# Kernel optimization log

Hardware: AMD Instinct MI355X
Metric: run time of the kernel (lower is better)

The kernel has to match this reference:

```python
import jax, jax.numpy as jnp
import numpy as np

EPS = 1e-5
NUM_HEADS = 16
HEAD_DIM = 128


def setup_inputs() -> dict:
    key = jax.random.key(0)
    ks = jax.random.split(key, 9)
    B, S, D = 2, 2048, 2048
    Hd2 = HEAD_DIM // 2
    # rotary angles: proper cos/sin of random phases (unit-modulus freqs_cis)
    theta = jax.random.uniform(ks[1], (B, S, Hd2), jnp.float32, 0.0, 2 * np.pi)
    return {
        "hidden_states": jax.random.normal(ks[0], (B, S, D), jnp.float32),
        "freqs_cos": jnp.cos(theta),
        "freqs_sin": jnp.sin(theta),
        "Wq": jax.random.normal(ks[2], (D, D), jnp.float32) * (D ** -0.5),
        "Wk": jax.random.normal(ks[3], (D, D), jnp.float32) * (D ** -0.5),
        "Wv": jax.random.normal(ks[4], (D, D), jnp.float32) * (D ** -0.5),
        "Wo": jax.random.normal(ks[5], (D, D), jnp.float32) * (D ** -0.5),
        "gq": jnp.ones((HEAD_DIM,), jnp.float32),
        "gk": jnp.ones((HEAD_DIM,), jnp.float32),
    }


def _rmsnorm(x, g):
    # normalize over last (head) dim, eps=1e-5, learned scale
    var = jnp.mean(jnp.square(x), axis=-1, keepdims=True)
    return x * jax.lax.rsqrt(var + EPS) * g


def _rope(x, cos, sin):
    # x: [B,S,H,hd]; treat last dim as hd/2 complex pairs; cos/sin: [B,S,hd/2]
    B, S, H, hd = x.shape
    xp = x.reshape(B, S, H, hd // 2, 2)
    xr, xi = xp[..., 0], xp[..., 1]
    c = cos[:, :, None, :]
    s = sin[:, :, None, :]
    out_r = xr * c - xi * s
    out_i = xr * s + xi * c
    return jnp.stack([out_r, out_i], axis=-1).reshape(B, S, H, hd)


def reference(hidden_states, freqs_cos, freqs_sin, Wq, Wk, Wv, Wo, gq, gk):
    B, S, D = hidden_states.shape
    H, hd = NUM_HEADS, HEAD_DIM
    q = (hidden_states @ Wq).reshape(B, S, H, hd)
    k = (hidden_states @ Wk).reshape(B, S, H, hd)
    v = (hidden_states @ Wv).reshape(B, S, H, hd)
    q = _rmsnorm(q, gq)
    k = _rmsnorm(k, gk)
    q = _rope(q, freqs_cos, freqs_sin)
    k = _rope(k, freqs_cos, freqs_sin)
    scale = 1.0 / np.sqrt(hd)
    scores = jnp.einsum("bqhd,bkhd->bhqk", q, k) * scale
    attn = jax.nn.softmax(scores, axis=-1)
    out = jnp.einsum("bhqk,bkhd->bqhd", attn, v)  # [B,S,H,hd]
    out = out.reshape(B, S, H * hd)
    return out @ Wo
```

## Files before the change

### kernel.cpp

```cpp
#include <hip/hip_runtime.h>
#include <hip/hip_bf16.h>

typedef __attribute__((ext_vector_type(8))) short bf16x8;
typedef __attribute__((ext_vector_type(4))) short bf16x4;
typedef __attribute__((ext_vector_type(4))) float f32x4;
typedef __attribute__((ext_vector_type(16))) float f32x16;
typedef __attribute__((ext_vector_type(4))) int   i32x4;
typedef __attribute__((ext_vector_type(2))) unsigned u32x2;
typedef __attribute__((ext_vector_type(4))) unsigned u32x4;

#define D_MODEL 2048
#define NTOK    4096
#define NH      16
#define HD      128
#define SEQ     2048
#define NQKV    6144

__device__ __forceinline__ short f2bf(float f) {
  unsigned u = __builtin_bit_cast(unsigned, f);
  unsigned r = u + 0x7FFFu + ((u >> 16) & 1u);
  return (short)(r >> 16);
}
__device__ __forceinline__ float bf2f(short s) {
  return __builtin_bit_cast(float, ((unsigned)(unsigned short)s) << 16);
}

__device__ __forceinline__ float exp2fast(float x) {
#if __has_builtin(__builtin_amdgcn_exp2f)
  return __builtin_amdgcn_exp2f(x);
#else
  return exp2f(x);
#endif
}

__device__ __forceinline__ unsigned cvt_pk_bf16(float a, float b) {
  unsigned r;
  asm("v_cvt_pk_bf16_f32 %0, %1, %2" : "=v"(r) : "v"(a), "v"(b));
  return r;
}

__device__ __forceinline__ void permswap(unsigned& x, unsigned& y) {
#if __has_builtin(__builtin_amdgcn_permlane32_swap)
  u32x2 r = __builtin_amdgcn_permlane32_swap(x, y, false, false);
  x = r[0]; y = r[1];
#else
  asm volatile("v_permlane32_swap_b32 %0, %1" : "+v"(x), "+v"(y));
#endif
}

__device__ __forceinline__ f32x16 mfma32(bf16x8 a, bf16x8 b, f32x16 c) {
  return __builtin_amdgcn_mfma_f32_32x32x16_bf16(a, b, c, 0, 0, 0);
}

__device__ __forceinline__ void gload_lds16(const void* g, void* l) {
  typedef __attribute__((address_space(1))) const unsigned gu32;
  typedef __attribute__((address_space(3))) unsigned lu32;
  __builtin_amdgcn_global_load_lds((gu32*)(uintptr_t)g,
                                   (lu32*)(unsigned)(uintptr_t)l, 16, 0, 0);
}

__global__ __launch_bounds__(256) void cast_bf16(const float* __restrict__ in,
                                                 short* __restrict__ out, int n4) {
  int i = blockIdx.x * 256 + threadIdx.x;
  if (i >= n4) return;
  float4 v = ((const float4*)in)[i];
  short4 o;
  o.x = f2bf(v.x); o.y = f2bf(v.y); o.z = f2bf(v.z); o.w = f2bf(v.w);
  ((short4*)out)[i] = o;
}

__global__ __launch_bounds__(256) void wtrans(const float* __restrict__ w0,
                                              const float* __restrict__ w1,
                                              const float* __restrict__ w2,
                                              const float* __restrict__ w3,
                                              short* __restrict__ wt) {
  int z = blockIdx.z;
  const float* W = (z == 0) ? w0 : (z == 1) ? w1 : (z == 2) ? w2 : w3;
  short* O = wt + (size_t)z * D_MODEL * D_MODEL;
  int n0 = blockIdx.x * 64, k0 = blockIdx.y * 64;
  __shared__ short T[64 * 136];
  int tid = threadIdx.x;
#pragma unroll
  for (int it = 0; it < 4; ++it) {
    int f = it * 256 + tid, kk = f >> 4, nc = f & 15;
    float4 v = *(const float4*)&W[(size_t)(k0 + kk) * D_MODEL + n0 + nc * 4];
    short4 o;
    o.x = f2bf(v.x); o.y = f2bf(v.y); o.z = f2bf(v.z); o.w = f2bf(v.w);
    *(short4*)&T[kk * 136 + nc * 4] = o;
  }
  __syncthreads();
#pragma unroll
  for (int it = 0; it < 4; ++it) {
    int u = it * 256 + tid, nn = u >> 4, kc = u & 15;
    short4 o;
    o.x = T[(kc * 4 + 0) * 136 + nn];
    o.y = T[(kc * 4 + 1) * 136 + nn];
    o.z = T[(kc * 4 + 2) * 136 + nn];
    o.w = T[(kc * 4 + 3) * 136 + nn];
    *(short4*)&O[(size_t)(n0 + nn) * D_MODEL + k0 + kc * 4] = o;
  }
}

template <bool OUTBF16>
__global__ __launch_bounds__(512, 4) void gemm8(const short* __restrict__ A,
                                                const short* __restrict__ Bt,
                                                void* __restrict__ Cv, int CS) {
  __shared__ short L[3 * 12288];
  int tid = threadIdx.x, w = tid >> 6, lane = tid & 63, c = lane & 15, g = lane >> 4;

  int gx = gridDim.x, gy = gridDim.y;
  int lin = blockIdx.x + gx * blockIdx.y;
  int idx = lin >> 3, nst = (gx * gy) >> 7;
  int s = (lin & 7) * nst + (idx >> 4);
  int w16 = idx & 15;
  int smR = gy >> 2;
  int mblk = (s % smR) * 4 + (w16 >> 2);
  int nblk = (s / smR) * 4 + (w16 & 3);
  int m0 = mblk * 256, n0 = nblk * 128;
  int wm = w >> 1, wn = w & 1;

  const int NKT = D_MODEL / 32;

  int asrc[2], bsrc;
#pragma unroll
  for (int q = 0; q < 2; ++q) {
    int o = (2 * w + q) * 1024 + lane * 16;
    int os = o ^ (((o >> 7) & 7) << 4);
    asrc[q] = (m0 + (os >> 6)) * D_MODEL + ((os & 63) >> 1);
  }
  {
    int o = w * 1024 + lane * 16;
    int os = o ^ (((o >> 7) & 7) << 4);
    bsrc = (n0 + (os >> 6)) * D_MODEL + ((os & 63) >> 1);
  }

  int aoff[4], boff[4];
#pragma unroll
  for (int mi = 0; mi < 4; ++mi) {
    int r = wm * 64 + mi * 16 + c;
    int o = r * 64 + g * 16;
    aoff[mi] = o ^ (((o >> 7) & 7) << 4);
  }
#pragma unroll
  for (int ni = 0; ni < 4; ++ni) {
    int r = wn * 64 + ni * 16 + c;
    int o = r * 64 + g * 16;
    boff[ni] = 16384 + (o ^ (((o >> 7) & 7) << 4));
  }

  auto STAGE = [&](int jt, int slot) {
    int kk = jt * 32;
    char* base = (char*)L + slot * 24576;
    gload_lds16(A + asrc[0] + kk, base + (2 * w) * 1024);
    gload_lds16(A + asrc[1] + kk, base + (2 * w + 1) * 1024);
    gload_lds16(Bt + bsrc + kk, base + 16384 + w * 1024);
  };

  f32x4 acc[4][4] = {};

  STAGE(0, 0); STAGE(1, 1);
  asm volatile("s_waitcnt vmcnt(3)" ::: "memory");
  __builtin_amdgcn_s_barrier();
  asm volatile("" ::: "memory");

  int rdslot = 0;
  for (int jt = 0; jt < NKT; ++jt) {
    int stslot = rdslot + 2; if (stslot >= 3) stslot -= 3;
    if (jt + 2 < NKT) STAGE(jt + 2, stslot);
    const char* buf = (const char*)L + rdslot * 24576;
    bf16x8 af[4], bfv[4];
#pragma unroll
    for (int mi = 0; mi < 4; ++mi) af[mi] = *(const bf16x8*)(buf + aoff[mi]);
#pragma unroll
    for (int ni = 0; ni < 4; ++ni) bfv[ni] = *(const bf16x8*)(buf + boff[ni]);
    __builtin_amdgcn_s_setprio(1);
#pragma unroll
    for (int mi = 0; mi < 4; ++mi)
#pragma unroll
      for (int ni = 0; ni < 4; ++ni)
        acc[mi][ni] = __builtin_amdgcn_mfma_f32_16x16x32_bf16(af[mi], bfv[ni],
                                                              acc[mi][ni], 0, 0, 0);
    __builtin_amdgcn_s_setprio(0);
    if (jt + 1 < NKT) {
      if (jt + 2 < NKT) { asm volatile("s_waitcnt vmcnt(3)" ::: "memory"); }
      else              { asm volatile("s_waitcnt vmcnt(0)" ::: "memory"); }
      __builtin_amdgcn_s_barrier();
      asm volatile("" ::: "memory");
    }
    rdslot = (rdslot == 2) ? 0 : rdslot + 1;
  }

  int row0 = m0 + wm * 64, col0 = n0 + wn * 64;
  if (OUTBF16) {
    short* Cb = (short*)Cv;
#pragma unroll
    for (int mi = 0; mi < 4; ++mi)
#pragma unroll
      for (int ni = 0; ni < 4; ++ni)
#pragma unroll
        for (int i = 0; i < 4; ++i)
          Cb[(size_t)(row0 + mi * 16 + g * 4 + i) * CS + col0 + ni * 16 + c] =
              f2bf(acc[mi][ni][i]);
  } else {
    float* Cf = (float*)Cv;
#pragma unroll
    for (int mi = 0; mi < 4; ++mi)
#pragma unroll
      for (int ni = 0; ni < 4; ++ni)
#pragma unroll
        for (int i = 0; i < 4; ++i)
          Cf[(size_t)(row0 + mi * 16 + g * 4 + i) * CS + col0 + ni * 16 + c] =
              acc[mi][ni][i];
  }
}

__global__ __launch_bounds__(256) void norm_rope(const short* __restrict__ qkv16,
                                                 const float* __restrict__ cosb,
                                                 const float* __restrict__ sinb,
                                                 const float* __restrict__ gq,
                                                 const float* __restrict__ gk,
                                                 short* __restrict__ qn,
                                                 short* __restrict__ kn) {
  int z = blockIdx.y;
  const float* gg = z ? gk : gq;
  short* O = z ? kn : qn;
  int w = threadIdx.x >> 6, lane = threadIdx.x & 63;
  int p = blockIdx.x * 4 + w;
  int token = p >> 4, h = p & 15;
  int v = *(const int*)&qkv16[(size_t)token * NQKV + z * D_MODEL + h * HD + lane * 2];
  float x0 = bf2f((short)(v & 0xffff));
  float x1 = bf2f((short)((unsigned)v >> 16));
  float ss = x0 * x0 + x1 * x1;
#pragma unroll
  for (int mk = 32; mk; mk >>= 1) ss += __shfl_xor(ss, mk);
  float rs = rsqrtf(ss * (1.f / 128.f) + 1e-5f);
  float qs = z ? 1.0f : 0.12751744f;
  rs *= qs;
  float xr = x0 * rs * gg[lane * 2];
  float xi = x1 * rs * gg[lane * 2 + 1];
  float cc = cosb[(size_t)token * 64 + lane];
  float sn = sinb[(size_t)token * 64 + lane];
  float or_ = xr * cc - xi * sn;
  float oi_ = xr * sn + xi * cc;
  int b = token >> 11, sidx = token & 2047;
  size_t dst = ((size_t)(b * NH + h) * SEQ + sidx) * HD + lane * 2;
  unsigned pk = (unsigned)(unsigned short)f2bf(or_) |
                ((unsigned)(unsigned short)f2bf(oi_) << 16);
  *(unsigned*)&O[dst] = pk;
}

__global__ __launch_bounds__(256) void vtrans(const short* __restrict__ qkv16,
                                              short* __restrict__ vt) {
  int st = blockIdx.x, bh = blockIdx.y;
  int b = bh >> 4, h = bh & 15;
  int t0 = b * SEQ + st * 64;
  __shared__ short Lt[64 * 136];
  int tid = threadIdx.x;
#pragma unroll
  for (int it = 0; it < 4; ++it) {
    int f = it * 256 + tid, tk = f >> 4, ch = f & 15;
    *(i32x4*)&Lt[tk * 136 + ch * 8] =
        *(const i32x4*)&qkv16[(size_t)(t0 + tk) * NQKV + 2 * D_MODEL + h * HD + ch * 8];
  }
  __syncthreads();
#pragma unroll
  for (int it = 0; it < 4; ++it) {
    int u = it * 256 + tid, d = u >> 3, kg = u & 7;
    bf16x8 o;
#pragma unroll
    for (int j = 0; j < 8; ++j) o[j] = Lt[(kg * 8 + j) * 136 + d];
    *(bf16x8*)&vt[(size_t)(bh * HD + d) * SEQ + st * 64 + kg * 8] = o;
  }
}

__global__ __launch_bounds__(512, 2) void flash(const short* __restrict__ qn,
                                                const short* __restrict__ kn,
                                                const short* __restrict__ vt,
                                                short* __restrict__ attn) {
  __shared__ short Ks[2][64 * 128];
  __shared__ short Vs[2][128 * 64];
  int tid = threadIdx.x, w = tid >> 6, lane = tid & 63;
  int q31 = lane & 31, hi = lane >> 5;

  int phys = blockIdx.x;
  int xcd = phys & 7, idx = phys >> 3;
  int bh = xcd * 4 + (idx >> 3);
  int qb = idx & 7;
  int q0 = qb * 256 + w * 32;

  const size_t base = (size_t)bh * SEQ * HD;
  const short* Kg = kn + base;
  const short* Vg = vt + base;

  bf16x8 qf[8];
#pragma unroll
  for (int s = 0; s < 8; ++s)
    qf[s] = *(const bf16x8*)&qn[base + (size_t)(q0 + q31) * HD + s * 16 + hi * 8];

  f32x16 acc[4] = {};
  float m_ = -1e30f, l_ = 0.f;

  int ksrc[2], vsrc[2];
#pragma unroll
  for (int p = 0; p < 2; ++p) {
    int ch = w * 2 + p;
    int o = ch * 1024 + lane * 16;
    int kr = o >> 8, kc = o & 255;
    ksrc[p] = kr * HD + ((kc ^ ((kr & 7) << 4)) >> 1);
    int vr = o >> 7, vc = o & 127;
    vsrc[p] = vr * SEQ + ((vc ^ ((vr & 7) << 4)) >> 1);
  }
  int swz = (q31 & 7) << 4;
  int koff[8], voff[4];
#pragma unroll
  for (int kf = 0; kf < 8; ++kf) koff[kf] = (kf * 32 + hi * 16) ^ swz;
#pragma unroll
  for (int kk = 0; kk < 4; ++kk) voff[kk] = (kk * 32 + hi * 16) ^ swz;
  int krow0 = q31 * 256, krow1 = (32 + q31) * 256;

#pragma unroll
  for (int p = 0; p < 2; ++p) {
    int ch = w * 2 + p;
    gload_lds16(Kg + ksrc[p], (char*)&Ks[0][0] + ch * 1024);
    gload_lds16(Vg + vsrc[p], (char*)&Vs[0][0] + ch * 1024);
  }

  const int NT = SEQ / 64;
  for (int t = 0; t < NT; ++t) {
    int cur = t & 1;
    __syncthreads();
    if (t + 1 < NT) {
      int k0n = (t + 1) * 64;
#pragma unroll
      for (int p = 0; p < 2; ++p) {
        int ch = w * 2 + p;
        gload_lds16(Kg + (size_t)k0n * HD + ksrc[p], (char*)&Ks[cur ^ 1][0] + ch * 1024);
        gload_lds16(Vg + k0n + vsrc[p],              (char*)&Vs[cur ^ 1][0] + ch * 1024);
      }
    }
    const char* Kb = (const char*)&Ks[cur][0];
    const char* Vb = (const char*)&Vs[cur][0];

    f32x16 s0 = {0,0,0,0,0,0,0,0,0,0,0,0,0,0,0,0};
    f32x16 s1 = {0,0,0,0,0,0,0,0,0,0,0,0,0,0,0,0};
    __builtin_amdgcn_s_setprio(1);
#pragma unroll
    for (int kf = 0; kf < 8; ++kf) {
      bf16x8 k0 = *(const bf16x8*)(Kb + krow0 + koff[kf]);
      s0 = mfma32(k0, qf[kf], s0);
      bf16x8 k1 = *(const bf16x8*)(Kb + krow1 + koff[kf]);
      s1 = mfma32(k1, qf[kf], s1);
    }
    __builtin_amdgcn_s_setprio(0);

    float p0 = -1e30f, p1 = -1e30f, p2 = -1e30f, p3 = -1e30f;
#pragma unroll
    for (int i = 0; i < 4; ++i) {
      p0 = fmaxf(p0, fmaxf(s0[i], s0[i + 4]));
      p1 = fmaxf(p1, fmaxf(s0[i + 8], s0[i + 12]));
      p2 = fmaxf(p2, fmaxf(s1[i], s1[i + 4]));
      p3 = fmaxf(p3, fmaxf(s1[i + 8], s1[i + 12]));
    }
    float pmax = fmaxf(fmaxf(p0, p1), fmaxf(p2, p3));
    pmax = fmaxf(pmax, __shfl_xor(pmax, 32));
    if (!__all(pmax <= m_ + 11.5f)) {
      float mn = fmaxf(m_, pmax);
      float al = exp2fast(m_ - mn);
      m_ = mn; l_ *= al;
#pragma unroll
      for (int db = 0; db < 4; ++db)
#pragma unroll
        for (int i = 0; i < 16; ++i) acc[db][i] *= al;
    }
    float r0 = 0.f, r1 = 0.f;
#pragma unroll
    for (int i = 0; i < 16; ++i) {
      float pa = exp2fast(s0[i] - m_); r0 += pa; s0[i] = pa;
      float pb = exp2fast(s1[i] - m_); r1 += pb; s1[i] = pb;
    }
    float r = r0 + r1;
    r += __shfl_xor(r, 32);
    l_ += r;

    __builtin_amdgcn_s_setprio(1);
#pragma unroll
    for (int kt = 0; kt < 2; ++kt) {
      const f32x16& sv = kt ? s1 : s0;
#pragma unroll
      for (int c2 = 0; c2 < 2; ++c2) {
        unsigned x0 = cvt_pk_bf16(sv[c2 * 8 + 0], sv[c2 * 8 + 1]);
        unsigned x1 = cvt_pk_bf16(sv[c2 * 8 + 2], sv[c2 * 8 + 3]);
        unsigned y0 = cvt_pk_bf16(sv[c2 * 8 + 4], sv[c2 * 8 + 5]);
        unsigned y1 = cvt_pk_bf16(sv[c2 * 8 + 6], sv[c2 * 8 + 7]);
        permswap(x0, y0);
        permswap(x1, y1);
        u32x4 pw = {x0, x1, y0, y1};
        bf16x8 pfrag = __builtin_bit_cast(bf16x8, pw);
        int vo = voff[kt * 2 + c2];
#pragma unroll
        for (int db = 0; db < 4; ++db) {
          bf16x8 va = *(const bf16x8*)(Vb + (db * 32 + q31) * 128 + vo);
          acc[db] = mfma32(va, pfrag, acc[db]);
        }
      }
    }
    __builtin_amdgcn_s_setprio(0);
  }

  int b = bh >> 4, h = bh & 15;
  float linv = 1.f / l_;
  size_t orow = (size_t)(b * SEQ + q0 + q31) * D_MODEL + h * HD;
#pragma unroll
  for (int db = 0; db < 4; ++db)
#pragma unroll
    for (int rg = 0; rg < 4; ++rg) {
      short4 o;
      o.x = f2bf(acc[db][rg * 4 + 0] * linv);
      o.y = f2bf(acc[db][rg * 4 + 1] * linv);
      o.z = f2bf(acc[db][rg * 4 + 2] * linv);
      o.w = f2bf(acc[db][rg * 4 + 3] * linv);
      *(short4*)&attn[orow + db * 32 + rg * 8 + hi * 4] = o;
    }
}

extern "C" void kernel_launch(void* const* d_in, const int* in_sizes, int n_in,
                              void* d_out, int out_size, void* d_ws, size_t ws_size,
                              hipStream_t stream) {
  const float* hs   = (const float*)d_in[0];
  const float* fcos = (const float*)d_in[1];
  const float* fsin = (const float*)d_in[2];
  const float* Wq   = (const float*)d_in[3];
  const float* Wk   = (const float*)d_in[4];
  const float* Wv   = (const float*)d_in[5];
  const float* Wo   = (const float*)d_in[6];
  const float* gq   = (const float*)d_in[7];
  const float* gk   = (const float*)d_in[8];

  char* ws = (char*)d_ws;
  short* hs16  = (short*)ws;
  short* Wt    = (short*)(ws + 16777216);
  short* qkv16 = (short*)(ws + 50331648);
  short* qn    = (short*)(ws + 100663296);
  short* kn    = (short*)(ws + 117440512);
  short* vt    = (short*)(ws + 134217728);
  short* attn16 = hs16;

  cast_bf16<<<8192, 256, 0, stream>>>(hs, hs16, NTOK * D_MODEL / 4);
  wtrans<<<dim3(32, 32, 4), 256, 0, stream>>>(Wq, Wk, Wv, Wo, Wt);
  gemm8<true><<<dim3(48, 16), 512, 0, stream>>>(hs16, Wt, qkv16, NQKV);
  norm_rope<<<dim3(16384, 2), 256, 0, stream>>>(qkv16, fcos, fsin, gq, gk, qn, kn);
  vtrans<<<dim3(32, 32), 256, 0, stream>>>(qkv16, vt);
  flash<<<dim3(256), 512, 0, stream>>>(qn, kn, vt, attn16);
  gemm8<false><<<dim3(16, 16), 512, 0, stream>>>(attn16,
                                                 Wt + (size_t)3 * D_MODEL * D_MODEL,
                                                 d_out, D_MODEL);
}
```

Before: 273.8 us.

## Add 4-wave 256x128 GEMM for QKV projection and halve flash block size

Adds a new gemm4 kernel that uses 4 waves per 256x128 output tile with BK=32 and a triple-buffered LDS pipeline. Each wave computes a 128x64 sub-tile with 16x16x32 MFMAs, and the kernel replaces gemm8 for the QKV projection. The flash-attention kernel now runs 4 waves per block covering 128 queries, on 512 blocks instead of 256, and each wave stages twice as many K/V chunks. The goal is better occupancy and scheduling on the compute-heavy QKV GEMM and attention. In exchange, each flash block reuses its K/V tiles across fewer queries, and the new GEMM holds large per-wave accumulators that add register pressure.

```diff
diff --git a/kernel.cpp b/kernel.cpp
--- a/kernel.cpp
+++ b/kernel.cpp
@@ -98,6 +98,117 @@
     o.z = T[(kc * 4 + 2) * 136 + nn];
     o.w = T[(kc * 4 + 3) * 136 + nn];
     *(short4*)&O[(size_t)(n0 + nn) * D_MODEL + k0 + kc * 4] = o;
+  }
+}
+
+template <bool OUTBF16>
+__global__ __launch_bounds__(256, 2) void gemm4(const short* __restrict__ A,
+                                                const short* __restrict__ Bt,
+                                                void* __restrict__ Cv, int CS) {
+  __shared__ char L[3 * 24576];
+  int tid = threadIdx.x, w = tid >> 6, lane = tid & 63, c = lane & 15, g = lane >> 4;
+
+  int gx = gridDim.x, gy = gridDim.y;
+  int lin = blockIdx.x + gx * blockIdx.y;
+  int idx = lin >> 3, nst = (gx * gy) >> 7;
+  int s = (lin & 7) * nst + (idx >> 4);
+  int w16 = idx & 15;
+  int smR = gy >> 2;
+  int mblk = (s % smR) * 4 + (w16 >> 2);
+  int nblk = (s / smR) * 4 + (w16 & 3);
+  int m0 = mblk * 256, n0 = nblk * 128;
+  int wm = w >> 1, wn = w & 1;
+
+  const int NKT = D_MODEL / 32;
+
+  const short* gsrc[6];
+  int ldst[6];
+#pragma unroll
+  for (int j = 0; j < 6; ++j) {
+    int ch = w * 6 + j;
+    int o = (ch < 16 ? ch * 1024 : (ch - 16) * 1024) + lane * 16;
+    int os = o ^ (((o >> 7) & 7) << 4);
+    gsrc[j] = (ch < 16) ? A + (size_t)(m0 + (os >> 6)) * D_MODEL + ((os & 63) >> 1)
+                        : Bt + (size_t)(n0 + (os >> 6)) * D_MODEL + ((os & 63) >> 1);
+    ldst[j] = (ch < 16) ? ch * 1024 : 16384 + (ch - 16) * 1024;
+  }
+
+  int aoff[8], boff[4];
+#pragma unroll
+  for (int mi = 0; mi < 8; ++mi) {
+    int r = wm * 128 + mi * 16 + c;
+    int o = r * 64 + g * 16;
+    aoff[mi] = o ^ (((o >> 7) & 7) << 4);
+  }
+#pragma unroll
+  for (int ni = 0; ni < 4; ++ni) {
+    int r = wn * 64 + ni * 16 + c;
+    int o = r * 64 + g * 16;
+    boff[ni] = 16384 + (o ^ (((o >> 7) & 7) << 4));
+  }
+
+  auto STAGE = [&](int jt, int slot) {
+    int kk = jt * 32;
+    char* base = L + slot * 24576;
+#pragma unroll
+    for (int j = 0; j < 6; ++j) gload_lds16(gsrc[j] + kk, base + ldst[j]);
+  };
+
+  f32x4 acc[8][4] = {};
+
+  STAGE(0, 0); STAGE(1, 1);
+  asm volatile("s_waitcnt vmcnt(6)" ::: "memory");
+  __builtin_amdgcn_s_barrier();
+  asm volatile("" ::: "memory");
+
+  int rdslot = 0;
+  for (int jt = 0; jt < NKT; ++jt) {
+    int stslot = rdslot + 2; if (stslot >= 3) stslot -= 3;
+    if (jt + 2 < NKT) STAGE(jt + 2, stslot);
+    const char* buf = L + rdslot * 24576;
+    bf16x8 af[8], bfv[4];
+#pragma unroll
+    for (int mi = 0; mi < 8; ++mi) af[mi] = *(const bf16x8*)(buf + aoff[mi]);
+#pragma unroll
+    for (int ni = 0; ni < 4; ++ni) bfv[ni] = *(const bf16x8*)(buf + boff[ni]);
+    __builtin_amdgcn_s_setprio(1);
+#pragma unroll
+    for (int mi = 0; mi < 8; ++mi)
+#pragma unroll
+      for (int ni = 0; ni < 4; ++ni)
+        acc[mi][ni] = __builtin_amdgcn_mfma_f32_16x16x32_bf16(af[mi], bfv[ni],
+                                                              acc[mi][ni], 0, 0, 0);
+    __builtin_amdgcn_s_setprio(0);
+    if (jt + 1 < NKT) {
+      if (jt + 2 < NKT) { asm volatile("s_waitcnt vmcnt(6)" ::: "memory"); }
+      else              { asm volatile("s_waitcnt vmcnt(0)" ::: "memory"); }
+      __builtin_amdgcn_s_barrier();
+      asm volatile("" ::: "memory");
+    }
+    rdslot = (rdslot == 2) ? 0 : rdslot + 1;
+  }
+
+  int row0 = m0 + wm * 128, col0 = n0 + wn * 64;
+  if (OUTBF16) {
+    short* Cb = (short*)Cv;
+#pragma unroll
+    for (int mi = 0; mi < 8; ++mi)
+#pragma unroll
+      for (int ni = 0; ni < 4; ++ni)
+#pragma unroll
+        for (int i = 0; i < 4; ++i)
+          Cb[(size_t)(row0 + mi * 16 + g * 4 + i) * CS + col0 + ni * 16 + c] =
+              f2bf(acc[mi][ni][i]);
+  } else {
+    float* Cf = (float*)Cv;
+#pragma unroll
+    for (int mi = 0; mi < 8; ++mi)
+#pragma unroll
+      for (int ni = 0; ni < 4; ++ni)
+#pragma unroll
+        for (int i = 0; i < 4; ++i)
+          Cf[(size_t)(row0 + mi * 16 + g * 4 + i) * CS + col0 + ni * 16 + c] =
+              acc[mi][ni][i];
   }
 }
 
@@ -273,7 +384,7 @@
   }
 }
 
-__global__ __launch_bounds__(512, 2) void flash(const short* __restrict__ qn,
+__global__ __launch_bounds__(256, 2) void flash(const short* __restrict__ qn,
                                                 const short* __restrict__ kn,
                                                 const short* __restrict__ vt,
                                                 short* __restrict__ attn) {
@@ -284,9 +395,9 @@
 
   int phys = blockIdx.x;
   int xcd = phys & 7, idx = phys >> 3;
-  int bh = xcd * 4 + (idx >> 3);
-  int qb = idx & 7;
-  int q0 = qb * 256 + w * 32;
+  int bh = xcd * 4 + (idx >> 4);
+  int qb = idx & 15;
+  int q0 = qb * 128 + w * 32;
 
   const size_t base = (size_t)bh * SEQ * HD;
   const short* Kg = kn + base;
@@ -300,10 +411,10 @@
   f32x16 acc[4] = {};
   float m_ = -1e30f, l_ = 0.f;
 
-  int ksrc[2], vsrc[2];
-#pragma unroll
-  for (int p = 0; p < 2; ++p) {
-    int ch = w * 2 + p;
+  int ksrc[4], vsrc[4];
+#pragma unroll
+  for (int p = 0; p < 4; ++p) {
+    int ch = w * 4 + p;
     int o = ch * 1024 + lane * 16;
     int kr = o >> 8, kc = o & 255;
     ksrc[p] = kr * HD + ((kc ^ ((kr & 7) << 4)) >> 1);
@@ -319,8 +430,8 @@
   int krow0 = q31 * 256, krow1 = (32 + q31) * 256;
 
 #pragma unroll
-  for (int p = 0; p < 2; ++p) {
-    int ch = w * 2 + p;
+  for (int p = 0; p < 4; ++p) {
+    int ch = w * 4 + p;
     gload_lds16(Kg + ksrc[p], (char*)&Ks[0][0] + ch * 1024);
     gload_lds16(Vg + vsrc[p], (char*)&Vs[0][0] + ch * 1024);
   }
@@ -332,8 +443,8 @@
     if (t + 1 < NT) {
       int k0n = (t + 1) * 64;
 #pragma unroll
-      for (int p = 0; p < 2; ++p) {
-        int ch = w * 2 + p;
+      for (int p = 0; p < 4; ++p) {
+        int ch = w * 4 + p;
         gload_lds16(Kg + (size_t)k0n * HD + ksrc[p], (char*)&Ks[cur ^ 1][0] + ch * 1024);
         gload_lds16(Vg + k0n + vsrc[p],              (char*)&Vs[cur ^ 1][0] + ch * 1024);
       }
@@ -447,10 +558,10 @@
 
   cast_bf16<<<8192, 256, 0, stream>>>(hs, hs16, NTOK * D_MODEL / 4);
   wtrans<<<dim3(32, 32, 4), 256, 0, stream>>>(Wq, Wk, Wv, Wo, Wt);
-  gemm8<true><<<dim3(48, 16), 512, 0, stream>>>(hs16, Wt, qkv16, NQKV);
+  gemm4<true><<<dim3(48, 16), 256, 0, stream>>>(hs16, Wt, qkv16, NQKV);
   norm_rope<<<dim3(16384, 2), 256, 0, stream>>>(qkv16, fcos, fsin, gq, gk, qn, kn);
   vtrans<<<dim3(32, 32), 256, 0, stream>>>(qkv16, vt);
-  flash<<<dim3(256), 512, 0, stream>>>(qn, kn, vt, attn16);
+  flash<<<dim3(512), 256, 0, stream>>>(qn, kn, vt, attn16);
   gemm8<false><<<dim3(16, 16), 512, 0, stream>>>(attn16,
                                                  Wt + (size_t)3 * D_MODEL * D_MODEL,
                                                  d_out, D_MODEL);
```

After: 278.4 us. No clear change (+1.7%).
